# Kernel tuning notes

Hardware: AMD Instinct MI355X
Metric: run time of the kernel (lower is better)

The kernel has to match this reference:

```python
import jax, jax.numpy as jnp
import numpy as np

B, S, H, NH, SPAN = 1, 2048, 768, 12, 512
D = H // NH
EPS = 1e-7
SCALE_FACTOR = 3  # 1 + len([c2p, p2c]) per DeBERTa


def setup_inputs() -> dict:
    key = jax.random.key(0)
    ks = jax.random.split(key, 10)
    r = lambda i, shape, s=0.02: jax.random.normal(ks[i], shape, jnp.float32) * s
    return dict(
        hidden_states=jax.random.normal(ks[0], (B, S, H), jnp.float32),
        attention_mask=jnp.ones((B, S), jnp.int32),
        Wq=r(1, (H, H)), bq=jnp.zeros((H,), jnp.float32),
        Wk=r(2, (H, H)), bk=jnp.zeros((H,), jnp.float32),
        Wv=r(3, (H, H)), bv=jnp.zeros((H,), jnp.float32),
        rel_embeddings=r(4, (2 * SPAN, H), 1.0),
        Wpk=r(5, (H, H)),
        Wpq=r(6, (H, H)), bpq=jnp.zeros((H,), jnp.float32),
        Wo=r(7, (H, H)), bo=jnp.zeros((H,), jnp.float32),
        ln_gamma=jnp.ones((H,), jnp.float32),
        ln_beta=jnp.zeros((H,), jnp.float32),
    )


def _heads(x):
    # [B,S,H] -> [B,NH,S,D]
    return x.reshape(B, S, NH, D).transpose(0, 2, 1, 3)


def reference(hidden_states, attention_mask, Wq, bq, Wk, bk, Wv, bv,
              rel_embeddings, Wpk, Wpq, bpq, Wo, bo, ln_gamma, ln_beta):
    q = _heads(hidden_states @ Wq + bq)
    k = _heads(hidden_states @ Wk + bk)
    v = _heads(hidden_states @ Wv + bv)
    scale = 1.0 / jnp.sqrt(jnp.asarray(D * SCALE_FACTOR, jnp.float32))

    # content-to-content
    scores = jnp.einsum('bhid,bhjd->bhij', q, k) * scale

    # relative positions: rel[i,j] = i - j
    ids = jnp.arange(S)
    rel = ids[:, None] - ids[None, :]                       # [S,S]

    pos_k = (rel_embeddings @ Wpk).reshape(2 * SPAN, NH, D)        # [2L,h,d]
    pos_q = (rel_embeddings @ Wpq + bpq).reshape(2 * SPAN, NH, D)  # [2L,h,d]

    # content-to-position: gather over clamped relative index
    c2p = jnp.einsum('bhid,lhd->bhil', q, pos_k) * scale    # [B,h,S,2L]
    c2p_idx = jnp.clip(rel + SPAN, 0, 2 * SPAN - 1)         # [S,S]
    c2p_att = c2p[:, :, ids[:, None], c2p_idx]              # [B,h,S,S]

    # position-to-content: gather then transpose (DeBERTa)
    p2c = jnp.einsum('bhjd,lhd->bhjl', k, pos_q) * scale    # [B,h,S,2L]
    p2c_idx = jnp.clip(-rel + SPAN, 0, 2 * SPAN - 1)        # [S,S]
    p2c_att = jnp.swapaxes(p2c[:, :, ids[:, None], p2c_idx], -1, -2)

    scores = scores + c2p_att + p2c_att

    mask4 = (attention_mask[:, None, None, :] * attention_mask[:, None, :, None]).astype(bool)
    scores = jnp.where(mask4, scores, jnp.finfo(scores.dtype).min)
    probs = jax.nn.softmax(scores, axis=-1)

    ctx = jnp.einsum('bhij,bhjd->bhid', probs, v).transpose(0, 2, 1, 3).reshape(B, S, H)

    # BertSelfOutput: dense + (dropout=identity) + residual + LayerNorm
    out = ctx @ Wo + bo + hidden_states
    mu = out.mean(-1, keepdims=True)
    var = out.var(-1, keepdims=True)
    return (out - mu) / jnp.sqrt(var + EPS) * ln_gamma + ln_beta
```

## Files before the change

kernel.cpp:

```cpp
#include <hip/hip_runtime.h>
#include <hip/hip_bf16.h>


typedef short v8s __attribute__((ext_vector_type(8)));
typedef short v4s __attribute__((ext_vector_type(4)));
typedef float v4f __attribute__((ext_vector_type(4)));

__device__ __forceinline__ float b2f(unsigned short u) {
    union { unsigned int i; float f; } v; v.i = ((unsigned int)u) << 16; return v.f;
}
__device__ __forceinline__ unsigned short f2b(float f) {
    union { float f; unsigned int i; } v; v.f = f;
    unsigned int x = v.i;
    return (unsigned short)((x + 0x7FFFu + ((x >> 16) & 1u)) >> 16);
}

#define SEQ 2048
#define HD  768
#define NH_ 12
#define DH  64

struct WtArgs { const float* src[6]; unsigned short* dst[6]; };
__global__ void prep_kernel(WtArgs args, const float* __restrict__ hs,
                            const float* __restrict__ rel,
                            const float* __restrict__ bq, const float* __restrict__ bk,
                            const float* __restrict__ bv, const float* __restrict__ bpq,
                            unsigned short* __restrict__ Xb, unsigned short* __restrict__ Rb,
                            float* __restrict__ bias3, float* __restrict__ bias2) {
    const int z = blockIdx.z;
    const int tx = threadIdx.x, ty = threadIdx.y;
    if (z < 6) {
        __shared__ float tile[32][33];
        const float* Sp = args.src[z];
        unsigned short* Dp = args.dst[z];
        const int bx = blockIdx.x * 32, by = blockIdx.y * 32;
#pragma unroll
        for (int r = 0; r < 32; r += 8) tile[ty + r][tx] = Sp[(by + ty + r) * HD + bx + tx];
        __syncthreads();
#pragma unroll
        for (int r = 0; r < 32; r += 8) Dp[(bx + ty + r) * HD + by + tx] = f2b(tile[tx][ty + r]);
    } else {
        const long n1 = (long)SEQ * HD;
        const long n2 = 1024l * HD;
        const long N = n1 + n2 + 3840;
        const long stride = 24l * 24 * 256;
        long i = ((long)blockIdx.y * 24 + blockIdx.x) * 256 + ty * 32 + tx;
        for (; i < N; i += stride) {
            if (i < n1) Xb[i] = f2b(hs[i]);
            else if (i < n1 + n2) Rb[i - n1] = f2b(rel[i - n1]);
            else {
                int j = (int)(i - n1 - n2);
                if (j < 768)        bias3[j] = bq[j];
                else if (j < 1536)  bias3[j] = bk[j - 768];
                else if (j < 2304)  bias3[j] = bv[j - 1536];
                else if (j < 3072)  bias2[j - 2304] = 0.0f;
                else                bias2[j - 2304] = bpq[j - 3072];
            }
        }
    }
}

template <int BIAS, int RESID, int OUTF32>
__device__ __forceinline__ void gemm_core(
    const unsigned short* __restrict__ A, int lda,
    const unsigned short* __restrict__ Bt, int ldb,
    void* __restrict__ Cv, int ldc,
    const float* __restrict__ bias, const float* __restrict__ resid,
    int K, int m0, int n0, unsigned short* As, unsigned short* Bs) {
    const int t = threadIdx.x;
    const int wave = t >> 6, lane = t & 63, quad = lane >> 4, l16 = lane & 15;
    const int wm = (wave >> 1) * 64, wn = (wave & 1) * 64;
    v4f acc[4][4];
    const v4f z4 = {0.f, 0.f, 0.f, 0.f};
#pragma unroll
    for (int i = 0; i < 4; i++)
#pragma unroll
        for (int j = 0; j < 4; j++) acc[i][j] = z4;

    const int srow = t >> 1, scol = (t & 1) * 32;
    const unsigned short* ga = A + (long)(m0 + srow) * lda + scol;
    const unsigned short* gb = Bt + (long)(n0 + srow) * ldb + scol;
    unsigned short* wa = &As[srow * 72 + scol];
    unsigned short* wb = &Bs[srow * 72 + scol];

    for (int k0 = 0; k0 < K; k0 += 64) {
        __syncthreads();
        v8s a0 = *(const v8s*)(ga + k0);
        v8s a1 = *(const v8s*)(ga + k0 + 8);
        v8s a2 = *(const v8s*)(ga + k0 + 16);
        v8s a3 = *(const v8s*)(ga + k0 + 24);
        v8s b0 = *(const v8s*)(gb + k0);
        v8s b1 = *(const v8s*)(gb + k0 + 8);
        v8s b2 = *(const v8s*)(gb + k0 + 16);
        v8s b3 = *(const v8s*)(gb + k0 + 24);
        *(v8s*)(wa) = a0; *(v8s*)(wa + 8) = a1; *(v8s*)(wa + 16) = a2; *(v8s*)(wa + 24) = a3;
        *(v8s*)(wb) = b0; *(v8s*)(wb + 8) = b1; *(v8s*)(wb + 16) = b2; *(v8s*)(wb + 24) = b3;
        __syncthreads();
#pragma unroll
        for (int ks = 0; ks < 2; ks++) {
            v8s af[4], bf[4];
#pragma unroll
            for (int mt = 0; mt < 4; mt++)
                af[mt] = *(const v8s*)&As[(wm + 16 * mt + l16) * 72 + ks * 32 + quad * 8];
#pragma unroll
            for (int nt = 0; nt < 4; nt++)
                bf[nt] = *(const v8s*)&Bs[(wn + 16 * nt + l16) * 72 + ks * 32 + quad * 8];
#pragma unroll
            for (int mt = 0; mt < 4; mt++)
#pragma unroll
                for (int nt = 0; nt < 4; nt++)
                    acc[mt][nt] = __builtin_amdgcn_mfma_f32_16x16x32_bf16(af[mt], bf[nt], acc[mt][nt], 0, 0, 0);
        }
    }
    float* Cf = (float*)Cv;
    unsigned short* Ch = (unsigned short*)Cv;
#pragma unroll
    for (int mt = 0; mt < 4; mt++) {
#pragma unroll
        for (int nt = 0; nt < 4; nt++) {
            const int gn = n0 + wn + 16 * nt + l16;
            float bv_ = 0.0f;
            if (BIAS) bv_ = bias[gn];
#pragma unroll
            for (int r = 0; r < 4; r++) {
                const int gm = m0 + wm + 16 * mt + quad * 4 + r;
                float v = acc[mt][nt][r];
                if (BIAS) v += bv_;
                if (RESID) v += resid[(long)gm * ldc + gn];
                if (OUTF32) Cf[(long)gm * ldc + gn] = v;
                else        Ch[(long)gm * ldc + gn] = f2b(v);
            }
        }
    }
}

__global__ __launch_bounds__(256) void gemm_qkvpos(
    const unsigned short* __restrict__ Xb, const unsigned short* __restrict__ Rb,
    const unsigned short* __restrict__ W3T, const unsigned short* __restrict__ Wp2T,
    const float* __restrict__ bias3, const float* __restrict__ bias2,
    unsigned short* __restrict__ qkv, unsigned short* __restrict__ pos2) {
    __shared__ unsigned short As[128 * 72];
    __shared__ unsigned short Bs[128 * 72];
    const int z = blockIdx.z;
    if (z < 3) {
        gemm_core<1, 0, 0>(Xb, 768, W3T + (long)z * 768 * 768, 768,
                           qkv + (long)z * 2048 * 768, 768, bias3 + z * 768, nullptr,
                           768, blockIdx.y * 128, blockIdx.x * 128, As, Bs);
    } else {
        if (blockIdx.y >= 8) return;
        const int w = z - 3;
        gemm_core<1, 0, 0>(Rb, 768, Wp2T + (long)w * 768 * 768, 768,
                           pos2 + (long)w * 1024 * 768, 768, bias2 + w * 768, nullptr,
                           768, blockIdx.y * 128, blockIdx.x * 128, As, Bs);
    }
}

__global__ __launch_bounds__(256) void gemm_band(
    const unsigned short* __restrict__ qkv, const unsigned short* __restrict__ pos2,
    unsigned short* __restrict__ c2p, unsigned short* __restrict__ p2c,
    const unsigned short* __restrict__ vsrc, unsigned short* __restrict__ vTs) {
    __shared__ unsigned short As[128 * 72];
    __shared__ unsigned short Bs[128 * 72];
    const int z = blockIdx.z;
    if (z < 24) {
        const unsigned short* A;
        const unsigned short* B;
        unsigned short* C;
        if (z < 12) {
            A = qkv + z * 64; B = pos2 + z * 64; C = c2p + (long)z * 2048 * 1024;
        } else {
            const int h = z - 12;
            A = qkv + 2048l * 768 + h * 64; B = pos2 + 1024l * 768 + h * 64;
            C = p2c + (long)h * 2048 * 1024;
        }
        gemm_core<0, 0, 0>(A, 768, B, 768, C, 1024, nullptr, nullptr,
                           64, blockIdx.y * 128, blockIdx.x * 128, As, Bs);
    } else {
        unsigned short (*tile)[33] = (unsigned short(*)[33])As;
        const int b = blockIdx.y * 8 + blockIdx.x;
        const int tx = threadIdx.x & 31, ty = threadIdx.x >> 5;
        for (int tid = b; tid < 1536; tid += 128) {
            const int cx = (tid % 24) * 32;
            const int ry = (tid / 24) * 32;
            __syncthreads();
#pragma unroll
            for (int r = 0; r < 32; r += 8)
                tile[ty + r][tx] = vsrc[(long)(ry + ty + r) * HD + cx + tx];
            __syncthreads();
#pragma unroll
            for (int r = 0; r < 32; r += 8)
                vTs[(long)(cx + ty + r) * SEQ + ry + tx] = tile[tx][ty + r];
        }
    }
}

__global__ __launch_bounds__(256) void gemm_out(
    const unsigned short* __restrict__ ctx, const unsigned short* __restrict__ WoT,
    const float* __restrict__ bo, const float* __restrict__ hidden,
    float* __restrict__ out_pre) {
    __shared__ unsigned short As[128 * 72];
    __shared__ unsigned short Bs[128 * 72];
    gemm_core<1, 1, 1>(ctx, 768, WoT, 768, out_pre, 768, bo, hidden,
                       768, blockIdx.y * 128, blockIdx.x * 128, As, Bs);
}

__device__ __forceinline__ void stage_window(const unsigned short* __restrict__ row,
                                             int D0, v8s& w0, v8s& w1) {
    if (D0 <= 0) {
        unsigned short v = row[0];
#pragma unroll
        for (int u = 0; u < 8; u++) { w0[u] = (short)v; w1[u] = (short)v; }
    } else if (D0 - 15 >= 1023) {
        unsigned short v = row[1023];
#pragma unroll
        for (int u = 0; u < 8; u++) { w0[u] = (short)v; w1[u] = (short)v; }
    } else if (D0 <= 1023 && D0 - 15 >= 0) {
        v8s x = *(const v8s*)(row + D0 - 7);
        v8s y = *(const v8s*)(row + D0 - 15);
#pragma unroll
        for (int u = 0; u < 8; u++) { w0[u] = x[7 - u]; w1[u] = y[7 - u]; }
    } else {
#pragma unroll
        for (int u = 0; u < 16; u++) {
            int d = D0 - u; d = d < 0 ? 0 : (d > 1023 ? 1023 : d);
            short v = (short)row[d];
            if (u < 8) w0[u] = v; else w1[u - 8] = v;
        }
    }
}

__global__ __launch_bounds__(256, 4) void flash_kernel(
    const unsigned short* __restrict__ qb, const unsigned short* __restrict__ kb,
    const unsigned short* __restrict__ vT, const unsigned short* __restrict__ c2p,
    const unsigned short* __restrict__ p2c, float* __restrict__ opart,
    float* __restrict__ lpart) {
    __shared__ unsigned short Kl[64 * 72];
    __shared__ unsigned short Vl[64 * 72];
    __shared__ unsigned short Pw[64 * 72];
    __shared__ unsigned short CwPl[64 * 72];
    const int h = blockIdx.y;
    const int i0 = blockIdx.x * 64;
    const int jc = blockIdx.z;
    const int jbase = jc * 512;
    const int t = threadIdx.x;
    const int wave = t >> 6, lane = t & 63, quad = lane >> 4, l16 = lane & 15;
    const float scale = 0.07216878364870322f;
    const v4f z4 = {0.f, 0.f, 0.f, 0.f};

    v8s qf[2];
    {
        const unsigned short* qp = qb + (long)(i0 + wave * 16 + l16) * HD + h * DH + quad * 8;
        qf[0] = *(const v8s*)qp;
        qf[1] = *(const v8s*)(qp + 32);
    }
    float l_lane[4] = {0.f, 0.f, 0.f, 0.f};
    v4f o_acc[4];
#pragma unroll
    for (int nt = 0; nt < 4; nt++) o_acc[nt] = z4;

    const int srow = t >> 2, scoff = (t & 3) * 16;
    const unsigned short* kbase = kb + (long)srow * HD + h * DH + scoff;
    const unsigned short* vbase = vT + (long)(h * DH + srow) * SEQ + scoff + jbase;
    unsigned short* wk = &Kl[srow * 72 + scoff];
    unsigned short* wv = &Vl[srow * 72 + scoff];
    unsigned short* wc = &CwPl[srow * 72 + scoff];
    unsigned short* wp = &Pw[srow * 72 + scoff];
    const unsigned short* c2prow = c2p + ((long)h * SEQ + i0 + srow) * 1024;
    const unsigned short* p2cb = p2c + (long)h * SEQ * 1024;

    v8s k0v, k1v, v0v, v1v, cw0, cw1, pw0, pw1;
    auto load_tile = [&](int j0l) {
        k0v = *(const v8s*)(kbase + (long)(jbase + j0l) * HD);
        k1v = *(const v8s*)(kbase + (long)(jbase + j0l) * HD + 8);
        v0v = *(const v8s*)(vbase + j0l);
        v1v = *(const v8s*)(vbase + j0l + 8);
        stage_window(c2prow, (i0 + srow) - (jbase + j0l) - scoff + 512, cw0, cw1);
        stage_window(p2cb + (long)(jbase + j0l + srow) * 1024,
                     (jbase + j0l + srow) - i0 - scoff + 512, pw0, pw1);
    };
    load_tile(0);

    for (int tt = 0; tt < 8; tt++) {
        __syncthreads();
        *(v8s*)wk = k0v; *(v8s*)(wk + 8) = k1v;
        *(v8s*)wv = v0v; *(v8s*)(wv + 8) = v1v;
        *(v8s*)wc = cw0; *(v8s*)(wc + 8) = cw1;
        *(v8s*)wp = pw0; *(v8s*)(wp + 8) = pw1;
        if (tt + 1 < 8) load_tile((tt + 1) * 64);
        __syncthreads();

        v4f s[4] = {z4, z4, z4, z4};
#pragma unroll
        for (int ks = 0; ks < 2; ks++)
#pragma unroll
            for (int nt = 0; nt < 4; nt++) {
                v8s bf = *(const v8s*)&Kl[(16 * nt + l16) * 72 + ks * 32 + quad * 8];
                s[nt] = __builtin_amdgcn_mfma_f32_16x16x32_bf16(qf[ks], bf, s[nt], 0, 0, 0);
            }
        float sm[4][4];
#pragma unroll
        for (int nt = 0; nt < 4; nt++) {
            v4s p4 = *(const v4s*)&Pw[(nt * 16 + l16) * 72 + wave * 16 + quad * 4];
#pragma unroll
            for (int r = 0; r < 4; r++) {
                float c2pv = b2f(CwPl[(wave * 16 + quad * 4 + r) * 72 + nt * 16 + l16]);
                float p = __expf((s[nt][r] + c2pv + b2f((unsigned short)p4[r])) * scale);
                sm[nt][r] = p;
                l_lane[r] += p;
            }
        }
#pragma unroll
        for (int nt = 0; nt < 4; nt++)
#pragma unroll
            for (int r = 0; r < 4; r++)
                CwPl[(wave * 16 + quad * 4 + r) * 72 + nt * 16 + l16] = f2b(sm[nt][r]);
        asm volatile("s_waitcnt lgkmcnt(0)" ::: "memory");
#pragma unroll
        for (int ks = 0; ks < 2; ks++) {
            v8s pf = *(const v8s*)&CwPl[(wave * 16 + l16) * 72 + ks * 32 + quad * 8];
#pragma unroll
            for (int nt = 0; nt < 4; nt++) {
                v8s vf = *(const v8s*)&Vl[(16 * nt + l16) * 72 + ks * 32 + quad * 8];
                o_acc[nt] = __builtin_amdgcn_mfma_f32_16x16x32_bf16(pf, vf, o_acc[nt], 0, 0, 0);
            }
        }
    }
    float* op = opart + (long)jc * SEQ * HD;
#pragma unroll
    for (int nt = 0; nt < 4; nt++) {
        const int d = nt * 16 + l16;
#pragma unroll
        for (int r = 0; r < 4; r++) {
            const int i = i0 + wave * 16 + quad * 4 + r;
            op[(long)i * HD + h * DH + d] = o_acc[nt][r];
        }
    }
#pragma unroll
    for (int r = 0; r < 4; r++) {
        float l = l_lane[r];
#pragma unroll
        for (int off = 1; off < 16; off <<= 1) l += __shfl_xor(l, off);
        l_lane[r] = l;
    }
    if (l16 == 0) {
#pragma unroll
        for (int r = 0; r < 4; r++) {
            const int i = i0 + wave * 16 + quad * 4 + r;
            lpart[((long)jc * NH_ + h) * SEQ + i] = l_lane[r];
        }
    }
}

__global__ __launch_bounds__(256) void combine_kernel(const float* __restrict__ opart,
                                                      const float* __restrict__ lpart,
                                                      unsigned short* __restrict__ ctx) {
    const long idx = (long)blockIdx.x * 256 + threadIdx.x;
    const int i = (int)(idx / HD);
    const int hd = (int)(idx % HD);
    const int h = hd >> 6;
    float num = 0.f, den = 0.f;
#pragma unroll
    for (int c = 0; c < 4; c++) {
        num += opart[(long)c * SEQ * HD + idx];
        den += lpart[((long)c * NH_ + h) * SEQ + i];
    }
    ctx[idx] = f2b(num / den);
}

__global__ __launch_bounds__(256) void ln_kernel(const float* __restrict__ x,
                                                 const float* __restrict__ gamma,
                                                 const float* __restrict__ beta,
                                                 float* __restrict__ out) {
    const int row = blockIdx.x;
    const int t = threadIdx.x;
    const float* xr = x + (long)row * HD;
    float v0 = xr[t], v1 = xr[t + 256], v2 = xr[t + 512];
    float s = v0 + v1 + v2;
    float ss = v0 * v0 + v1 * v1 + v2 * v2;
#pragma unroll
    for (int off = 1; off < 64; off <<= 1) { s += __shfl_xor(s, off); ss += __shfl_xor(ss, off); }
    __shared__ float red[8];
    const int wave = t >> 6;
    if ((t & 63) == 0) { red[wave] = s; red[wave + 4] = ss; }
    __syncthreads();
    float S = red[0] + red[1] + red[2] + red[3];
    float SS = red[4] + red[5] + red[6] + red[7];
    const float inv = 1.0f / 768.0f;
    float mu = S * inv;
    float var = SS * inv - mu * mu;
    float rstd = rsqrtf(var + 1e-7f);
    float* orow = out + (long)row * HD;
    orow[t]       = (v0 - mu) * rstd * gamma[t]       + beta[t];
    orow[t + 256] = (v1 - mu) * rstd * gamma[t + 256] + beta[t + 256];
    orow[t + 512] = (v2 - mu) * rstd * gamma[t + 512] + beta[t + 512];
}

extern "C" void kernel_launch(void* const* d_in, const int* in_sizes, int n_in,
                              void* d_out, int out_size, void* d_ws, size_t ws_size,
                              hipStream_t stream) {
    const float* hidden = (const float*)d_in[0];
    const float* Wq  = (const float*)d_in[2];
    const float* bq  = (const float*)d_in[3];
    const float* Wk  = (const float*)d_in[4];
    const float* bk  = (const float*)d_in[5];
    const float* Wv  = (const float*)d_in[6];
    const float* bv  = (const float*)d_in[7];
    const float* rel = (const float*)d_in[8];
    const float* Wpk = (const float*)d_in[9];
    const float* Wpq = (const float*)d_in[10];
    const float* bpq = (const float*)d_in[11];
    const float* Wo  = (const float*)d_in[12];
    const float* bo  = (const float*)d_in[13];
    const float* gamma = (const float*)d_in[14];
    const float* beta  = (const float*)d_in[15];

    char* ws = (char*)d_ws;
    size_t off = 0;
    auto alloc = [&](size_t bytes) -> char* { char* p = ws + off; off += bytes; return p; };
    unsigned short* Xb   = (unsigned short*)alloc(2048ul * 768 * 2);
    unsigned short* Rb   = (unsigned short*)alloc(1024ul * 768 * 2);
    unsigned short* W3T  = (unsigned short*)alloc(3ul * 768 * 768 * 2);
    unsigned short* WoT  = (unsigned short*)alloc(768ul * 768 * 2);
    unsigned short* Wp2T = (unsigned short*)alloc(2ul * 768 * 768 * 2);
    float*          bias3 = (float*)alloc(2304 * 4);
    float*          bias2 = (float*)alloc(1536 * 4);
    unsigned short* qkv  = (unsigned short*)alloc(3ul * 2048 * 768 * 2);
    unsigned short* vTs  = (unsigned short*)alloc(768ul * 2048 * 2);
    unsigned short* pos2 = (unsigned short*)alloc(2ul * 1024 * 768 * 2);
    unsigned short* c2p  = (unsigned short*)alloc(12ul * 2048 * 1024 * 2);
    unsigned short* p2c  = (unsigned short*)alloc(12ul * 2048 * 1024 * 2);
    unsigned short* ctx  = (unsigned short*)alloc(2048ul * 768 * 2);
    float*          out_pre = (float*)alloc(2048ul * 768 * 4);
    float*          opart   = (float*)alloc(4ul * 2048 * 768 * 4);
    float*          lpart   = (float*)alloc(4ul * 12 * 2048 * 4);
    (void)ws_size;

    WtArgs wa;
    wa.src[0] = Wq;  wa.dst[0] = W3T;
    wa.src[1] = Wk;  wa.dst[1] = W3T + 768 * 768;
    wa.src[2] = Wv;  wa.dst[2] = W3T + 2 * 768 * 768;
    wa.src[3] = Wo;  wa.dst[3] = WoT;
    wa.src[4] = Wpk; wa.dst[4] = Wp2T;
    wa.src[5] = Wpq; wa.dst[5] = Wp2T + 768 * 768;
    prep_kernel<<<dim3(24, 24, 7), dim3(32, 8), 0, stream>>>(
        wa, hidden, rel, bq, bk, bv, bpq, Xb, Rb, bias3, bias2);

    gemm_qkvpos<<<dim3(6, 16, 5), 256, 0, stream>>>(Xb, Rb, W3T, Wp2T, bias3, bias2, qkv, pos2);
    gemm_band<<<dim3(8, 16, 25), 256, 0, stream>>>(qkv, pos2, c2p, p2c,
                                                   qkv + 2ul * 2048 * 768, vTs);
    flash_kernel<<<dim3(32, 12, 4), 256, 0, stream>>>(qkv, qkv + 2048ul * 768, vTs, c2p, p2c,
                                                      opart, lpart);
    combine_kernel<<<6144, 256, 0, stream>>>(opart, lpart, ctx);
    gemm_out<<<dim3(6, 16), 256, 0, stream>>>(ctx, WoT, bo, hidden, out_pre);
    ln_kernel<<<2048, 256, 0, stream>>>(out_pre, gamma, beta, (float*)d_out);
}
```

Baseline: 239.6 us.

## Fuse split-K combine into output GEMM and shrink GEMM tiles for occupancy

Removes the separate combine kernel and the bf16 ctx buffer. The output-projection GEMM now builds its A tile on the fly by summing the four opart partials and dividing by the summed lpart denominators. The GEMM core is templated on tile size: QKV/pos GEMMs move to 64x128 tiles and the output GEMM to 64x64 tiles, giving more blocks to fill the GPU's CUs. In exchange, the output GEMM re-reads the fp32 partials once per N-tile, which adds redundant global traffic.

```diff
diff --git a/kernel.cpp b/kernel.cpp
--- a/kernel.cpp
+++ b/kernel.cpp
@@ -60,64 +60,104 @@
     }
 }
 
-template <int BIAS, int RESID, int OUTF32>
+template <int TM, int TN, int CTXA, int BIAS, int RESID, int OUTF32>
 __device__ __forceinline__ void gemm_core(
     const unsigned short* __restrict__ A, int lda,
     const unsigned short* __restrict__ Bt, int ldb,
     void* __restrict__ Cv, int ldc,
     const float* __restrict__ bias, const float* __restrict__ resid,
+    const float* __restrict__ opart, const float* __restrict__ lpart,
     int K, int m0, int n0, unsigned short* As, unsigned short* Bs) {
+    constexpr int MT = TM / 32, NT = TN / 32;
     const int t = threadIdx.x;
     const int wave = t >> 6, lane = t & 63, quad = lane >> 4, l16 = lane & 15;
-    const int wm = (wave >> 1) * 64, wn = (wave & 1) * 64;
-    v4f acc[4][4];
+    const int wm = (wave & 1) * (TM / 2), wn = (wave >> 1) * (TN / 2);
+    v4f acc[MT][NT];
     const v4f z4 = {0.f, 0.f, 0.f, 0.f};
 #pragma unroll
-    for (int i = 0; i < 4; i++)
-#pragma unroll
-        for (int j = 0; j < 4; j++) acc[i][j] = z4;
-
-    const int srow = t >> 1, scol = (t & 1) * 32;
-    const unsigned short* ga = A + (long)(m0 + srow) * lda + scol;
-    const unsigned short* gb = Bt + (long)(n0 + srow) * ldb + scol;
-    unsigned short* wa = &As[srow * 72 + scol];
-    unsigned short* wb = &Bs[srow * 72 + scol];
+    for (int i = 0; i < MT; i++)
+#pragma unroll
+        for (int j = 0; j < NT; j++) acc[i][j] = z4;
+
+    const int arow = (TM == 128) ? (t >> 1) : (t >> 2);
+    const int acol = (TM == 128) ? ((t & 1) * 32) : ((t & 3) * 16);
+    const int brow = (TN == 128) ? (t >> 1) : (t >> 2);
+    const int bcol = (TN == 128) ? ((t & 1) * 32) : ((t & 3) * 16);
+    const unsigned short* ga = A + (long)(m0 + arow) * lda + acol;
+    const unsigned short* gb = Bt + (long)(n0 + brow) * ldb + bcol;
+    unsigned short* wa = &As[arow * 72 + acol];
+    unsigned short* wb = &Bs[brow * 72 + bcol];
 
     for (int k0 = 0; k0 < K; k0 += 64) {
         __syncthreads();
-        v8s a0 = *(const v8s*)(ga + k0);
-        v8s a1 = *(const v8s*)(ga + k0 + 8);
-        v8s a2 = *(const v8s*)(ga + k0 + 16);
-        v8s a3 = *(const v8s*)(ga + k0 + 24);
-        v8s b0 = *(const v8s*)(gb + k0);
-        v8s b1 = *(const v8s*)(gb + k0 + 8);
-        v8s b2 = *(const v8s*)(gb + k0 + 16);
-        v8s b3 = *(const v8s*)(gb + k0 + 24);
-        *(v8s*)(wa) = a0; *(v8s*)(wa + 8) = a1; *(v8s*)(wa + 16) = a2; *(v8s*)(wa + 24) = a3;
-        *(v8s*)(wb) = b0; *(v8s*)(wb + 8) = b1; *(v8s*)(wb + 16) = b2; *(v8s*)(wb + 24) = b3;
+        if constexpr (CTXA) {
+            const int i = m0 + arow;
+            const int h = k0 >> 6;
+            float den = 0.f;
+#pragma unroll
+            for (int c = 0; c < 4; c++) den += lpart[((long)c * NH_ + h) * SEQ + i];
+            const float inv = 1.0f / den;
+            v8s pk0, pk1;
+#pragma unroll
+            for (int g = 0; g < 4; g++) {
+                v4f s = z4;
+#pragma unroll
+                for (int c = 0; c < 4; c++)
+                    s += *(const v4f*)(opart + (long)c * SEQ * HD + (long)i * HD + k0 + acol + g * 4);
+#pragma unroll
+                for (int u = 0; u < 4; u++) {
+                    short v = (short)f2b(s[u] * inv);
+                    if (g < 2) pk0[g * 4 + u] = v; else pk1[(g - 2) * 4 + u] = v;
+                }
+            }
+            *(v8s*)wa = pk0; *(v8s*)(wa + 8) = pk1;
+        } else if constexpr (TM == 128) {
+            v8s a0 = *(const v8s*)(ga + k0);
+            v8s a1 = *(const v8s*)(ga + k0 + 8);
+            v8s a2 = *(const v8s*)(ga + k0 + 16);
+            v8s a3 = *(const v8s*)(ga + k0 + 24);
+            *(v8s*)(wa) = a0; *(v8s*)(wa + 8) = a1;
+            *(v8s*)(wa + 16) = a2; *(v8s*)(wa + 24) = a3;
+        } else {
+            v8s a0 = *(const v8s*)(ga + k0);
+            v8s a1 = *(const v8s*)(ga + k0 + 8);
+            *(v8s*)(wa) = a0; *(v8s*)(wa + 8) = a1;
+        }
+        if constexpr (TN == 128) {
+            v8s b0 = *(const v8s*)(gb + k0);
+            v8s b1 = *(const v8s*)(gb + k0 + 8);
+            v8s b2 = *(const v8s*)(gb + k0 + 16);
+            v8s b3 = *(const v8s*)(gb + k0 + 24);
+            *(v8s*)(wb) = b0; *(v8s*)(wb + 8) = b1;
+            *(v8s*)(wb + 16) = b2; *(v8s*)(wb + 24) = b3;
+        } else {
+            v8s b0 = *(const v8s*)(gb + k0);
+            v8s b1 = *(const v8s*)(gb + k0 + 8);
+            *(v8s*)(wb) = b0; *(v8s*)(wb + 8) = b1;
+        }
         __syncthreads();
 #pragma unroll
         for (int ks = 0; ks < 2; ks++) {
-            v8s af[4], bf[4];
-#pragma unroll
-            for (int mt = 0; mt < 4; mt++)
+            v8s af[MT], bf[NT];
+#pragma unroll
+            for (int mt = 0; mt < MT; mt++)
                 af[mt] = *(const v8s*)&As[(wm + 16 * mt + l16) * 72 + ks * 32 + quad * 8];
 #pragma unroll
-            for (int nt = 0; nt < 4; nt++)
+            for (int nt = 0; nt < NT; nt++)
                 bf[nt] = *(const v8s*)&Bs[(wn + 16 * nt + l16) * 72 + ks * 32 + quad * 8];
 #pragma unroll
-            for (int mt = 0; mt < 4; mt++)
-#pragma unroll
-                for (int nt = 0; nt < 4; nt++)
+            for (int mt = 0; mt < MT; mt++)
+#pragma unroll
+                for (int nt = 0; nt < NT; nt++)
                     acc[mt][nt] = __builtin_amdgcn_mfma_f32_16x16x32_bf16(af[mt], bf[nt], acc[mt][nt], 0, 0, 0);
         }
     }
     float* Cf = (float*)Cv;
     unsigned short* Ch = (unsigned short*)Cv;
 #pragma unroll
-    for (int mt = 0; mt < 4; mt++) {
-#pragma unroll
-        for (int nt = 0; nt < 4; nt++) {
+    for (int mt = 0; mt < MT; mt++) {
+#pragma unroll
+        for (int nt = 0; nt < NT; nt++) {
             const int gn = n0 + wn + 16 * nt + l16;
             float bv_ = 0.0f;
             if (BIAS) bv_ = bias[gn];
@@ -139,19 +179,20 @@
     const unsigned short* __restrict__ W3T, const unsigned short* __restrict__ Wp2T,
     const float* __restrict__ bias3, const float* __restrict__ bias2,
     unsigned short* __restrict__ qkv, unsigned short* __restrict__ pos2) {
-    __shared__ unsigned short As[128 * 72];
+    __shared__ unsigned short As[64 * 72];
     __shared__ unsigned short Bs[128 * 72];
     const int z = blockIdx.z;
+    const int m0 = blockIdx.y * 64, n0 = blockIdx.x * 128;
     if (z < 3) {
-        gemm_core<1, 0, 0>(Xb, 768, W3T + (long)z * 768 * 768, 768,
-                           qkv + (long)z * 2048 * 768, 768, bias3 + z * 768, nullptr,
-                           768, blockIdx.y * 128, blockIdx.x * 128, As, Bs);
+        gemm_core<64, 128, 0, 1, 0, 0>(Xb, 768, W3T + (long)z * 768 * 768, 768,
+                                       qkv + (long)z * 2048 * 768, 768, bias3 + z * 768,
+                                       nullptr, nullptr, nullptr, 768, m0, n0, As, Bs);
     } else {
-        if (blockIdx.y >= 8) return;
+        if (blockIdx.y >= 16) return;
         const int w = z - 3;
-        gemm_core<1, 0, 0>(Rb, 768, Wp2T + (long)w * 768 * 768, 768,
-                           pos2 + (long)w * 1024 * 768, 768, bias2 + w * 768, nullptr,
-                           768, blockIdx.y * 128, blockIdx.x * 128, As, Bs);
+        gemm_core<64, 128, 0, 1, 0, 0>(Rb, 768, Wp2T + (long)w * 768 * 768, 768,
+                                       pos2 + (long)w * 1024 * 768, 768, bias2 + w * 768,
+                                       nullptr, nullptr, nullptr, 768, m0, n0, As, Bs);
     }
 }
 
@@ -173,8 +214,9 @@
             A = qkv + 2048l * 768 + h * 64; B = pos2 + 1024l * 768 + h * 64;
             C = p2c + (long)h * 2048 * 1024;
         }
-        gemm_core<0, 0, 0>(A, 768, B, 768, C, 1024, nullptr, nullptr,
-                           64, blockIdx.y * 128, blockIdx.x * 128, As, Bs);
+        gemm_core<128, 128, 0, 0, 0, 0>(A, 768, B, 768, C, 1024, nullptr, nullptr,
+                                        nullptr, nullptr, 64,
+                                        blockIdx.y * 128, blockIdx.x * 128, As, Bs);
     } else {
         unsigned short (*tile)[33] = (unsigned short(*)[33])As;
         const int b = blockIdx.y * 8 + blockIdx.x;
@@ -195,13 +237,15 @@
 }
 
 __global__ __launch_bounds__(256) void gemm_out(
-    const unsigned short* __restrict__ ctx, const unsigned short* __restrict__ WoT,
+    const float* __restrict__ opart, const float* __restrict__ lpart,
+    const unsigned short* __restrict__ WoT,
     const float* __restrict__ bo, const float* __restrict__ hidden,
     float* __restrict__ out_pre) {
-    __shared__ unsigned short As[128 * 72];
-    __shared__ unsigned short Bs[128 * 72];
-    gemm_core<1, 1, 1>(ctx, 768, WoT, 768, out_pre, 768, bo, hidden,
-                       768, blockIdx.y * 128, blockIdx.x * 128, As, Bs);
+    __shared__ unsigned short As[64 * 72];
+    __shared__ unsigned short Bs[64 * 72];
+    gemm_core<64, 64, 1, 1, 1, 1>(nullptr, 768, WoT, 768, out_pre, 768, bo, hidden,
+                                  opart, lpart, 768,
+                                  blockIdx.y * 64, blockIdx.x * 64, As, Bs);
 }
 
 __device__ __forceinline__ void stage_window(const unsigned short* __restrict__ row,
@@ -349,22 +393,6 @@
             lpart[((long)jc * NH_ + h) * SEQ + i] = l_lane[r];
         }
     }
-}
-
-__global__ __launch_bounds__(256) void combine_kernel(const float* __restrict__ opart,
-                                                      const float* __restrict__ lpart,
-                                                      unsigned short* __restrict__ ctx) {
-    const long idx = (long)blockIdx.x * 256 + threadIdx.x;
-    const int i = (int)(idx / HD);
-    const int hd = (int)(idx % HD);
-    const int h = hd >> 6;
-    float num = 0.f, den = 0.f;
-#pragma unroll
-    for (int c = 0; c < 4; c++) {
-        num += opart[(long)c * SEQ * HD + idx];
-        den += lpart[((long)c * NH_ + h) * SEQ + i];
-    }
-    ctx[idx] = f2b(num / den);
 }
 
 __global__ __launch_bounds__(256) void ln_kernel(const float* __restrict__ x,
@@ -429,7 +457,6 @@
     unsigned short* pos2 = (unsigned short*)alloc(2ul * 1024 * 768 * 2);
     unsigned short* c2p  = (unsigned short*)alloc(12ul * 2048 * 1024 * 2);
     unsigned short* p2c  = (unsigned short*)alloc(12ul * 2048 * 1024 * 2);
-    unsigned short* ctx  = (unsigned short*)alloc(2048ul * 768 * 2);
     float*          out_pre = (float*)alloc(2048ul * 768 * 4);
     float*          opart   = (float*)alloc(4ul * 2048 * 768 * 4);
     float*          lpart   = (float*)alloc(4ul * 12 * 2048 * 4);
@@ -445,12 +472,11 @@
     prep_kernel<<<dim3(24, 24, 7), dim3(32, 8), 0, stream>>>(
         wa, hidden, rel, bq, bk, bv, bpq, Xb, Rb, bias3, bias2);
 
-    gemm_qkvpos<<<dim3(6, 16, 5), 256, 0, stream>>>(Xb, Rb, W3T, Wp2T, bias3, bias2, qkv, pos2);
+    gemm_qkvpos<<<dim3(6, 32, 5), 256, 0, stream>>>(Xb, Rb, W3T, Wp2T, bias3, bias2, qkv, pos2);
     gemm_band<<<dim3(8, 16, 25), 256, 0, stream>>>(qkv, pos2, c2p, p2c,
                                                    qkv + 2ul * 2048 * 768, vTs);
     flash_kernel<<<dim3(32, 12, 4), 256, 0, stream>>>(qkv, qkv + 2048ul * 768, vTs, c2p, p2c,
                                                       opart, lpart);
-    combine_kernel<<<6144, 256, 0, stream>>>(opart, lpart, ctx);
-    gemm_out<<<dim3(6, 16), 256, 0, stream>>>(ctx, WoT, bo, hidden, out_pre);
+    gemm_out<<<dim3(12, 32), 256, 0, stream>>>(opart, lpart, WoT, bo, hidden, out_pre);
     ln_kernel<<<2048, 256, 0, stream>>>(out_pre, gamma, beta, (float*)d_out);
 }
```

New measurement: 261.4 us. 9.1% more time.
